# Kernel tuning notes

Hardware: AMD Instinct MI355X
Metric: run time of the kernel (lower is better)

The kernel has to match this reference:

```python
import jax, jax.numpy as jnp
import numpy as np
import math

D_MODEL = 1024
N_HEADS = 16
D_HEAD = D_MODEL // N_HEADS
NUM_BUCKETS = 32
MAX_DISTANCE = 128
B, LQ, LK = 2, 2048, 2048


def _rel_pos_bucket(rel):
    # rel: [Lq, Lk] int32, rel = mem - ctx
    n = jnp.clip(-rel, 0, None)
    max_exact = NUM_BUCKETS // 2
    is_small = n < max_exact
    val_if_large = max_exact + (
        jnp.log(n.astype(jnp.float32) / max_exact + 1e-9)
        / math.log(MAX_DISTANCE / max_exact)
        * (NUM_BUCKETS - max_exact)
    ).astype(jnp.int32)
    val_if_large = jnp.minimum(val_if_large, NUM_BUCKETS - 1)
    return jnp.where(is_small, n, val_if_large)


def setup_inputs() -> dict:
    key = jax.random.key(0)
    ks = jax.random.split(key, 9)
    scale = 1.0 / math.sqrt(D_MODEL)
    q = jax.random.normal(ks[0], (B, LQ, D_MODEL), dtype=jnp.float32)
    k = jax.random.normal(ks[1], (B, LK, D_MODEL), dtype=jnp.float32)
    v = jax.random.normal(ks[2], (B, LK, D_MODEL), dtype=jnp.float32)
    key_padding_mask = jax.random.randint(ks[3], (B, 1, 1, LK), 0, 2).astype(bool)
    Wq = jax.random.normal(ks[4], (D_MODEL, D_MODEL), dtype=jnp.float32) * scale
    Wk = jax.random.normal(ks[5], (D_MODEL, D_MODEL), dtype=jnp.float32) * scale
    Wv = jax.random.normal(ks[6], (D_MODEL, D_MODEL), dtype=jnp.float32) * scale
    Wo = jax.random.normal(ks[7], (D_MODEL, D_MODEL), dtype=jnp.float32) * scale
    rel_emb = jax.random.normal(ks[8], (NUM_BUCKETS, N_HEADS), dtype=jnp.float32) * 0.02
    return {"q": q, "k": k, "v": v, "key_padding_mask": key_padding_mask,
            "Wq": Wq, "Wk": Wk, "Wv": Wv, "Wo": Wo, "rel_emb": rel_emb}


def reference(q, k, v, key_padding_mask, Wq, Wk, Wv, Wo, rel_emb):
    Bq, Lq, _ = q.shape
    Lk = k.shape[1]
    # projections (nn.Linear: x @ W.T), split heads -> [B, H, L, dh]
    qh = (q @ Wq.T).reshape(Bq, Lq, N_HEADS, D_HEAD).transpose(0, 2, 1, 3)
    kh = (k @ Wk.T).reshape(Bq, Lk, N_HEADS, D_HEAD).transpose(0, 2, 1, 3)
    vh = (v @ Wv.T).reshape(Bq, Lk, N_HEADS, D_HEAD).transpose(0, 2, 1, 3)
    scores = jnp.einsum('bhqd,bhkd->bhqk', qh, kh) / math.sqrt(D_HEAD)
    # relative position bias: [1, H, Lq, Lk]
    rel = jnp.arange(Lk, dtype=jnp.int32)[None, :] - jnp.arange(Lq, dtype=jnp.int32)[:, None]
    buckets = _rel_pos_bucket(rel)  # [Lq, Lk]
    bias = rel_emb[buckets]         # [Lq, Lk, H]
    scores = scores + bias.transpose(2, 0, 1)[None]
    scores = jnp.where(key_padding_mask, scores, -1e9)
    attn = jax.nn.softmax(scores, axis=-1)
    out = jnp.einsum('bhqk,bhkd->bhqd', attn, vh)
    out = out.transpose(0, 2, 1, 3).reshape(Bq, Lq, D_MODEL)
    return out @ Wo.T
```

## Files before the change

kernel.cpp:

```cpp
#include <hip/hip_runtime.h>
#include <math.h>

typedef _Float16 f16;
typedef __fp16 h16x2 __attribute__((ext_vector_type(2)));
typedef _Float16 f16x4 __attribute__((ext_vector_type(4)));
typedef _Float16 f16x8 __attribute__((ext_vector_type(8)));
typedef float f32x4 __attribute__((ext_vector_type(4)));
typedef float f32x16 __attribute__((ext_vector_type(16)));
typedef unsigned int u32;

#define D_MODEL 1024
#define NHEADS 16
#define DHEAD 64
#define LQ 2048
#define LKK 2048
#define BB 2
#define LOG2E 1.4426950408889634f

static __device__ __forceinline__ void gload16(const void* g, void* l) {
  __builtin_amdgcn_global_load_lds(
      (const __attribute__((address_space(1))) u32*)g,
      (__attribute__((address_space(3))) u32*)l, 16, 0, 0);
}
static __device__ __forceinline__ float ex2(float x) {
  float r;
  asm volatile("v_exp_f32 %0, %1\n\ts_nop 0" : "=v"(r) : "v"(x));
  return r;
}
static __device__ __forceinline__ u32 pkr(float a, float b) {
  union { h16x2 h; u32 u; } c;
  c.h = __builtin_amdgcn_cvt_pkrtz(a, b);
  return c.u;
}
#define MFMA16(a, b, c) __builtin_amdgcn_mfma_f32_16x16x32_f16(a, b, c, 0, 0, 0)
#define MFMA32(a, b, c) __builtin_amdgcn_mfma_f32_32x32x16_f16(a, b, c, 0, 0, 0)

__global__ void k_prep(const void* msk, const float* __restrict__ rel,
                       float* __restrict__ biasT, unsigned char* __restrict__ m8) {
  __shared__ int o1s, o2s;
  const int t = threadIdx.x;
  if (t == 0) { o1s = 0; o2s = 0; }
  __syncthreads();
  const unsigned char* raw = (const unsigned char*)msk;
  int o1 = 0, o2 = 0;
  for (int i = t; i < BB * LKK; i += 256) {
    unsigned char vv = raw[i];
    if ((i & 3) && vv) o1 = 1;
    if (((i & 3) == 2) && vv == 0x80u) o2 = 1;
  }
  if (o1) atomicOr(&o1s, 1);
  if (o2) atomicOr(&o2s, 1);
  __syncthreads();
  const int f = o1s ? (o2s ? 2 : 1) : 0;
  for (int i = t; i < BB * LKK; i += 256) {
    unsigned char v;
    if (f == 0)      v = (((const int*)msk)[i] != 0);
    else if (f == 1) v = (((const unsigned char*)msk)[i] != 0);
    else             v = (((const float*)msk)[i] != 0.0f);
    m8[i] = v;
  }
  for (int n = t; n < 2048; n += 256) {
    int bucket;
    if (n < 16) bucket = n;
    else {
      float tt = logf((float)n / 16.0f + 1e-9f);
      tt = tt / 2.0794415416798357f;
      tt = tt * 16.0f;
      bucket = 16 + (int)tt;
      if (bucket > 31) bucket = 31;
    }
    for (int h = 0; h < NHEADS; ++h)
      biasT[h * 2048 + n] = rel[bucket * NHEADS + h] * LOG2E;
  }
}

__global__ void k_cvt_all(const float* q, const float* k, const float* v,
                          const float* Wq, const float* Wk, const float* Wv, const float* Wo,
                          f16* Xq, f16* Xk, f16* Xv, f16* W16) {
  int i = blockIdx.x * 256 + threadIdx.x;
  const float* s; f16* d; int off;
  if (i < 3145728) {
    int which = i >> 20; off = i & 1048575;
    s = which == 0 ? q : (which == 1 ? k : v);
    d = which == 0 ? Xq : (which == 1 ? Xk : Xv);
  } else {
    int j = i - 3145728; int which = j >> 18; off = j & 262143;
    s = which == 0 ? Wq : (which == 1 ? Wk : (which == 2 ? Wv : Wo));
    d = W16 + which * 1048576;
  }
  float4 x = ((const float4*)s)[off];
  f16x4 o; o[0] = (f16)x.x; o[1] = (f16)x.y; o[2] = (f16)x.z; o[3] = (f16)x.w;
  ((f16x4*)d)[off] = o;
}

template <int EPI>
static __device__ __forceinline__ void gemm_core(const f16* __restrict__ A,
                                                 const f16* __restrict__ Bm,
                                                 void* __restrict__ C) {
  __shared__ __align__(16) f16 sA[128 * 32];
  __shared__ __align__(16) f16 sB[128 * 32];
  const int t = threadIdx.x;
  const int w = t >> 6, lane = t & 63;
  const int lg = lane >> 4, lc = lane & 15;
  const int wr = w >> 1, wc = w & 1;
  const long row0 = (long)blockIdx.x * 128;
  const long col0 = (long)blockIdx.y * 128;
  f32x4 acc[4][4] = {};

  for (int kk = 0; kk < 1024; kk += 32) {
#pragma unroll
    for (int it = 0; it < 2; ++it) {
      int ch = t + it * 256;
      int r = ch >> 2, kg = ch & 3;
      gload16(A + (row0 + r) * 1024 + kk + kg * 8, (char*)sA + ch * 16);
      gload16(Bm + (col0 + r) * 1024 + kk + kg * 8, (char*)sB + ch * 16);
    }
    __syncthreads();
    f16x8 af[4], bf[4];
#pragma unroll
    for (int i = 0; i < 4; ++i)
      af[i] = *(const f16x8*)&sA[(wr * 64 + i * 16 + lc) * 32 + lg * 8];
#pragma unroll
    for (int j = 0; j < 4; ++j)
      bf[j] = *(const f16x8*)&sB[(wc * 64 + j * 16 + lc) * 32 + lg * 8];
#pragma unroll
    for (int i = 0; i < 4; ++i)
#pragma unroll
      for (int j = 0; j < 4; ++j)
        acc[i][j] = MFMA16(af[i], bf[j], acc[i][j]);
    __syncthreads();
  }
#pragma unroll
  for (int i = 0; i < 4; ++i)
#pragma unroll
    for (int j = 0; j < 4; ++j)
#pragma unroll
      for (int r = 0; r < 4; ++r) {
        long row = row0 + wr * 64 + i * 16 + lg * 4 + r;
        long col = col0 + wc * 64 + j * 16 + lc;
        float v = acc[i][j][r];
        if (EPI == 0) {
          long b = row >> 11, l = row & 2047;
          long h = col >> 6, d = col & 63;
          ((f16*)C)[(((b * NHEADS + h) * LQ) + l) * DHEAD + d] = (f16)v;
        } else {
          ((float*)C)[row * 1024 + col] = v;
        }
      }
}

__global__ void __launch_bounds__(256, 2)
k_gemm_qkv(const f16* __restrict__ Xq, const f16* __restrict__ Xk, const f16* __restrict__ Xv,
           const f16* __restrict__ W16, f16* __restrict__ QHp, f16* __restrict__ KHp,
           f16* __restrict__ VHp, int zoff) {
  const int z = blockIdx.z + zoff;
  const f16* A = z == 0 ? Xq : (z == 1 ? Xk : Xv);
  const f16* Bm = W16 + (size_t)z * 1048576;
  f16* C = z == 0 ? QHp : (z == 1 ? KHp : VHp);
  gemm_core<0>(A, Bm, C);
}

__global__ void __launch_bounds__(256, 2)
k_gemm_o(const f16* __restrict__ A, const f16* __restrict__ Bm, float* __restrict__ C) {
  gemm_core<1>(A, Bm, C);
}

__global__ void __launch_bounds__(256, 2)
k_attn(const f16* __restrict__ QH, const f16* __restrict__ KH, const f16* __restrict__ VH,
       const float* __restrict__ BIASg, const unsigned char* __restrict__ M8,
       f16* __restrict__ O16) {
  __shared__ __align__(16) f16 sK[2][64 * 64];
  __shared__ __align__(16) f16 sVT[2][64 * 64];
  __shared__ __align__(16) float sBias[4104];
  __shared__ __align__(16) float sPen[2048];

  const int L = blockIdx.x;
  const int bh = (L & 7) * 4 + ((L >> 3) & 3);
  const int qc = L >> 5;
  const int b = bh >> 4, h = bh & 15;
  const int t = threadIdx.x, w = t >> 6, lane = t & 63;
  const int lq = lane & 31;
  const int hi = lane >> 5;
  const int q0w = qc * 128 + w * 32;
  const size_t base = (size_t)bh * LKK * DHEAD;

  for (int i = t; i < 4104; i += 256) {
    int n = i - 2052; n = n < 0 ? 0 : (n > 2047 ? 2047 : n);
    sBias[i] = BIASg[h * 2048 + n];
  }
  for (int i = t; i < 2048; i += 256)
    sPen[i] = M8[b * LKK + i] ? 0.0f : -3.0e9f;

  f16x8 qb[4];
  const f16* qrow = QH + base + (size_t)(q0w + lq) * DHEAD;
#pragma unroll
  for (int s = 0; s < 4; ++s)
    qb[s] = *(const f16x8*)(qrow + s * 16 + hi * 8);

  auto STAGE = [&](int kt, int buf) {
#pragma unroll
    for (int it = 0; it < 2; ++it) {
      int ch = t + it * 256;
      int r = ch >> 3, g = ch & 7;
      gload16(KH + base + (size_t)(kt * 64 + r) * DHEAD + (g ^ (r & 7)) * 8,
              (char*)&sK[buf][0] + ch * 16);
    }
#pragma unroll
    for (int it = 0; it < 2; ++it) {
      int ch = t + it * 256;
      int kr = ch & 63, dg = ch >> 6;
      uint4 vv = *(const uint4*)(VH + base + (size_t)(kt * 64 + kr) * DHEAD + dg * 8);
      const f16* pv = (const f16*)&vv;
#pragma unroll
      for (int e = 0; e < 8; ++e) {
        int d = dg * 8 + e;
        *(f16*)((char*)&sVT[buf][0] + ((d * 128 + kr * 2) ^ ((d & 7) << 4))) = pv[e];
      }
    }
  };

  float m_r = -1e30f, l_r = 0.0f;
  f32x16 oacc0 = {}, oacc1 = {};
  const float c1 = 0.125f * LOG2E;

  STAGE(0, 0);
  __syncthreads();

  for (int kt = 0; kt < 32; ++kt) {
    const int cur = kt & 1;
    if (kt < 31) STAGE(kt + 1, cur ^ 1);

    f32x16 sa0 = {}, sa1 = {};
#pragma unroll
    for (int s = 0; s < 4; ++s) {
      f16x8 k0 = *(const f16x8*)((const char*)&sK[cur][0] +
                   ((lq * 128 + s * 32 + hi * 16) ^ ((lq & 7) << 4)));
      f16x8 k1 = *(const f16x8*)((const char*)&sK[cur][0] +
                   (((32 + lq) * 128 + s * 32 + hi * 16) ^ ((lq & 7) << 4)));
      sa0 = MFMA32(k0, qb[s], sa0);
      sa1 = MFMA32(k1, qb[s], sa1);
    }

    float p_[32];
#pragma unroll
    for (int r = 0; r < 16; ++r) { p_[r] = sa0[r]; p_[16 + r] = sa1[r]; }

#pragma unroll
    for (int u = 0; u < 8; ++u) {
      int tt = u >> 2, j = u & 3;
      int kbase = kt * 64 + tt * 32 + j * 8 + hi * 4;
      f32x4 pen4 = *(const f32x4*)&sPen[kbase];
      int bidx0 = (q0w + lq) - kbase + 2052;
#pragma unroll
      for (int e = 0; e < 4; ++e) {
        float bp = sBias[bidx0 - e] + pen4[e];
        int r = tt * 16 + j * 4 + e;
        p_[r] = p_[r] * c1 + bp;
      }
    }

    float tm[16];
#pragma unroll
    for (int r = 0; r < 16; ++r) tm[r] = fmaxf(p_[2 * r], p_[2 * r + 1]);
#pragma unroll
    for (int s = 8; s > 0; s >>= 1)
#pragma unroll
      for (int r = 0; r < s; ++r) tm[r] = fmaxf(tm[r], tm[r + s]);
    float mx = fmaxf(tm[0], __shfl_xor(tm[0], 32));

    if (__any(mx > m_r + 8.0f)) {
      float mnew = fmaxf(m_r, mx);
      float al = ex2(m_r - mnew);
      m_r = mnew; l_r *= al;
#pragma unroll
      for (int r = 0; r < 16; ++r) { oacc0[r] *= al; oacc1[r] *= al; }
    }

#pragma unroll
    for (int r = 0; r < 32; ++r) p_[r] = ex2(p_[r] - m_r);

    float ts[16];
#pragma unroll
    for (int r = 0; r < 16; ++r) ts[r] = p_[2 * r] + p_[2 * r + 1];
#pragma unroll
    for (int s = 8; s > 0; s >>= 1)
#pragma unroll
      for (int r = 0; r < s; ++r) ts[r] += ts[r + s];
    l_r += ts[0] + __shfl_xor(ts[0], 32);

    f16x8 pf[4];
#pragma unroll
    for (int sl = 0; sl < 4; ++sl) {
      int tt = sl >> 1, sp = sl & 1;
      int bA = tt * 16 + (2 * sp) * 4, bB = tt * 16 + (2 * sp + 1) * 4;
      u32 A0 = pkr(p_[bA], p_[bA + 1]);
      u32 A1 = pkr(p_[bA + 2], p_[bA + 3]);
      u32 B0 = pkr(p_[bB], p_[bB + 1]);
      u32 B1 = pkr(p_[bB + 2], p_[bB + 3]);
      asm volatile("v_permlane32_swap_b32 %0, %1" : "+v"(A0), "+v"(B0));
      asm volatile("v_permlane32_swap_b32 %0, %1" : "+v"(A1), "+v"(B1));
      union { u32 u[4]; f16x8 v; } c;
      c.u[0] = A0; c.u[1] = A1; c.u[2] = B0; c.u[3] = B1;
      pf[sl] = c.v;
    }

#pragma unroll
    for (int sl = 0; sl < 4; ++sl) {
      int K0 = sl * 16;
      f16x8 v0 = *(const f16x8*)((const char*)&sVT[cur][0] +
                   ((lq * 128 + K0 * 2 + hi * 16) ^ ((lq & 7) << 4)));
      f16x8 v1 = *(const f16x8*)((const char*)&sVT[cur][0] +
                   (((32 + lq) * 128 + K0 * 2 + hi * 16) ^ ((lq & 7) << 4)));
      oacc0 = MFMA32(v0, pf[sl], oacc0);
      oacc1 = MFMA32(v1, pf[sl], oacc1);
    }
    __syncthreads();
  }

  const float rinv = 1.0f / l_r;
  const size_t orow = ((size_t)b * LQ + (q0w + lq)) * D_MODEL + h * DHEAD;
#pragma unroll
  for (int dh = 0; dh < 2; ++dh)
#pragma unroll
    for (int j = 0; j < 4; ++j) {
      int d0 = dh * 32 + j * 8 + hi * 4;
      f16x4 ov;
#pragma unroll
      for (int e = 0; e < 4; ++e) {
        float x = (dh ? oacc1[j * 4 + e] : oacc0[j * 4 + e]) * rinv;
        ov[e] = (f16)x;
      }
      *(f16x4*)(O16 + orow + d0) = ov;
    }
}

extern "C" void kernel_launch(void* const* d_in, const int* in_sizes, int n_in,
                              void* d_out, int out_size, void* d_ws, size_t ws_size,
                              hipStream_t stream) {
  (void)in_sizes; (void)n_in; (void)out_size;
  const float* q   = (const float*)d_in[0];
  const float* k   = (const float*)d_in[1];
  const float* v   = (const float*)d_in[2];
  const void*  msk = d_in[3];
  const float* Wq  = (const float*)d_in[4];
  const float* Wk  = (const float*)d_in[5];
  const float* Wv  = (const float*)d_in[6];
  const float* Wo  = (const float*)d_in[7];
  const float* rel = (const float*)d_in[8];

  char* ws = (char*)d_ws;
  const size_t SL = (size_t)8 << 20;
  const bool bigA = ws_size >= 8 * SL;

  f16 *Xq, *Xk, *Xv, *QHp, *KHp, *VHp, *O16, *W16; char* misc;
  if (bigA) {
    Xq = (f16*)(ws + 0 * SL); Xk = (f16*)(ws + 1 * SL); Xv = (f16*)(ws + 2 * SL);
    QHp = (f16*)(ws + 3 * SL); KHp = (f16*)(ws + 4 * SL); VHp = (f16*)(ws + 5 * SL);
    W16 = (f16*)(ws + 6 * SL); O16 = (f16*)(ws + 2 * SL);
    misc = ws + 7 * SL;
  } else {
    Xq = (f16*)(ws + 0 * SL); Xk = (f16*)(ws + 1 * SL); Xv = (f16*)(ws + 2 * SL);
    QHp = (f16*)(ws + 3 * SL); KHp = (f16*)(ws + 0 * SL); VHp = (f16*)(ws + 1 * SL);
    W16 = (f16*)(ws + 4 * SL); O16 = (f16*)(ws + 2 * SL);
    misc = ws + 5 * SL;
  }
  float* BIAS = (float*)misc;
  unsigned char* M8 = (unsigned char*)(misc + (192 << 10));

  k_prep<<<1, 256, 0, stream>>>(msk, rel, BIAS, M8);
  k_cvt_all<<<16384, 256, 0, stream>>>(q, k, v, Wq, Wk, Wv, Wo, Xq, Xk, Xv, W16);

  if (bigA) {
    k_gemm_qkv<<<dim3(32, 8, 3), 256, 0, stream>>>(Xq, Xk, Xv, W16, QHp, KHp, VHp, 0);
  } else {
    for (int z = 0; z < 3; ++z)
      k_gemm_qkv<<<dim3(32, 8, 1), 256, 0, stream>>>(Xq, Xk, Xv, W16, QHp, KHp, VHp, z);
  }
  k_attn<<<512, 256, 0, stream>>>(QHp, KHp, VHp, BIAS, M8, O16);
  k_gemm_o<<<dim3(32, 8), 256, 0, stream>>>(O16, W16 + 3 * 1048576, (float*)d_out);
}
```

Baseline: 165.0 us.

## Write V projection pre-transposed and load it asynchronously into LDS

Result: faster. 155.1 us (-6.0%).

```diff
diff --git a/kernel.cpp b/kernel.cpp
--- a/kernel.cpp
+++ b/kernel.cpp
@@ -31,6 +31,9 @@
   union { h16x2 h; u32 u; } c;
   c.h = __builtin_amdgcn_cvt_pkrtz(a, b);
   return c.u;
+}
+static __device__ __forceinline__ float fmax3(float a, float b, float c) {
+  return fmaxf(fmaxf(a, b), c);
 }
 #define MFMA16(a, b, c) __builtin_amdgcn_mfma_f32_16x16x32_f16(a, b, c, 0, 0, 0)
 #define MFMA32(a, b, c) __builtin_amdgcn_mfma_f32_32x32x16_f16(a, b, c, 0, 0, 0)
@@ -133,31 +136,46 @@
 #pragma unroll
   for (int i = 0; i < 4; ++i)
 #pragma unroll
-    for (int j = 0; j < 4; ++j)
-#pragma unroll
-      for (int r = 0; r < 4; ++r) {
-        long row = row0 + wr * 64 + i * 16 + lg * 4 + r;
-        long col = col0 + wc * 64 + j * 16 + lc;
-        float v = acc[i][j][r];
-        if (EPI == 0) {
-          long b = row >> 11, l = row & 2047;
-          long h = col >> 6, d = col & 63;
-          ((f16*)C)[(((b * NHEADS + h) * LQ) + l) * DHEAD + d] = (f16)v;
-        } else {
-          ((float*)C)[row * 1024 + col] = v;
+    for (int j = 0; j < 4; ++j) {
+      const long rowb = row0 + wr * 64 + i * 16 + lg * 4;
+      const long col = col0 + wc * 64 + j * 16 + lc;
+      if (EPI == 2) {
+        long b = rowb >> 11, l0 = rowb & 2047;
+        long h = col >> 6, d = col & 63;
+        f16x4 ov;
+#pragma unroll
+        for (int r = 0; r < 4; ++r) ov[r] = (f16)acc[i][j][r];
+        *(f16x4*)((f16*)C + (((b * NHEADS + h) * DHEAD + d) * (long)LKK + l0)) = ov;
+      } else {
+#pragma unroll
+        for (int r = 0; r < 4; ++r) {
+          long row = rowb + r;
+          float v = acc[i][j][r];
+          if (EPI == 0) {
+            long b = row >> 11, l = row & 2047;
+            long h = col >> 6, d = col & 63;
+            ((f16*)C)[(((b * NHEADS + h) * LQ) + l) * DHEAD + d] = (f16)v;
+          } else {
+            ((float*)C)[row * 1024 + col] = v;
+          }
         }
       }
-}
-
-__global__ void __launch_bounds__(256, 2)
+    }
+}
+
+__global__ void __launch_bounds__(256, 3)
 k_gemm_qkv(const f16* __restrict__ Xq, const f16* __restrict__ Xk, const f16* __restrict__ Xv,
            const f16* __restrict__ W16, f16* __restrict__ QHp, f16* __restrict__ KHp,
-           f16* __restrict__ VHp, int zoff) {
+           f16* __restrict__ VTp, int zoff) {
   const int z = blockIdx.z + zoff;
-  const f16* A = z == 0 ? Xq : (z == 1 ? Xk : Xv);
-  const f16* Bm = W16 + (size_t)z * 1048576;
-  f16* C = z == 0 ? QHp : (z == 1 ? KHp : VHp);
-  gemm_core<0>(A, Bm, C);
+  if (z == 2) {
+    gemm_core<2>(Xv, W16 + 2 * 1048576, VTp);
+  } else {
+    const f16* A = z == 0 ? Xq : Xk;
+    const f16* Bm = W16 + (size_t)z * 1048576;
+    f16* C = z == 0 ? QHp : KHp;
+    gemm_core<0>(A, Bm, C);
+  }
 }
 
 __global__ void __launch_bounds__(256, 2)
@@ -166,7 +184,7 @@
 }
 
 __global__ void __launch_bounds__(256, 2)
-k_attn(const f16* __restrict__ QH, const f16* __restrict__ KH, const f16* __restrict__ VH,
+k_attn(const f16* __restrict__ QH, const f16* __restrict__ KH, const f16* __restrict__ VT,
        const float* __restrict__ BIASg, const unsigned char* __restrict__ M8,
        f16* __restrict__ O16) {
   __shared__ __align__(16) f16 sK[2][64 * 64];
@@ -197,31 +215,26 @@
   for (int s = 0; s < 4; ++s)
     qb[s] = *(const f16x8*)(qrow + s * 16 + hi * 8);
 
+  const int ch0 = t, ch1 = t + 256;
+  const int r0 = ch0 >> 3, g0 = ((ch0 & 7) ^ (r0 & 7)) * 8;
+  const int r1 = ch1 >> 3, g1 = ((ch1 & 7) ^ (r1 & 7)) * 8;
+  const f16* Kb = KH + base;
+  const f16* Vb = VT + base;
+
   auto STAGE = [&](int kt, int buf) {
-#pragma unroll
-    for (int it = 0; it < 2; ++it) {
-      int ch = t + it * 256;
-      int r = ch >> 3, g = ch & 7;
-      gload16(KH + base + (size_t)(kt * 64 + r) * DHEAD + (g ^ (r & 7)) * 8,
-              (char*)&sK[buf][0] + ch * 16);
-    }
-#pragma unroll
-    for (int it = 0; it < 2; ++it) {
-      int ch = t + it * 256;
-      int kr = ch & 63, dg = ch >> 6;
-      uint4 vv = *(const uint4*)(VH + base + (size_t)(kt * 64 + kr) * DHEAD + dg * 8);
-      const f16* pv = (const f16*)&vv;
-#pragma unroll
-      for (int e = 0; e < 8; ++e) {
-        int d = dg * 8 + e;
-        *(f16*)((char*)&sVT[buf][0] + ((d * 128 + kr * 2) ^ ((d & 7) << 4))) = pv[e];
-      }
-    }
+    const int k0 = kt * 64;
+    gload16(Kb + (size_t)(k0 + r0) * DHEAD + g0, (char*)&sK[buf][0] + ch0 * 16);
+    gload16(Kb + (size_t)(k0 + r1) * DHEAD + g1, (char*)&sK[buf][0] + ch1 * 16);
+    gload16(Vb + (size_t)r0 * LKK + k0 + g0, (char*)&sVT[buf][0] + ch0 * 16);
+    gload16(Vb + (size_t)r1 * LKK + k0 + g1, (char*)&sVT[buf][0] + ch1 * 16);
   };
 
-  float m_r = -1e30f, l_r = 0.0f;
-  f32x16 oacc0 = {}, oacc1 = {};
+  float m_r = -1e30f;
+  f32x16 oacc0 = {}, oacc1 = {}, oaccL = {};
   const float c1 = 0.125f * LOG2E;
+  f16x8 ones;
+#pragma unroll
+  for (int e = 0; e < 8; ++e) ones[e] = (f16)1.0f;
 
   STAGE(0, 0);
   __syncthreads();
@@ -259,34 +272,27 @@
       }
     }
 
-    float tm[16];
-#pragma unroll
-    for (int r = 0; r < 16; ++r) tm[r] = fmaxf(p_[2 * r], p_[2 * r + 1]);
-#pragma unroll
-    for (int s = 8; s > 0; s >>= 1)
-#pragma unroll
-      for (int r = 0; r < s; ++r) tm[r] = fmaxf(tm[r], tm[r + s]);
-    float mx = fmaxf(tm[0], __shfl_xor(tm[0], 32));
+    float mm[11];
+#pragma unroll
+    for (int r = 0; r < 10; ++r) mm[r] = fmax3(p_[3 * r], p_[3 * r + 1], p_[3 * r + 2]);
+    mm[10] = fmaxf(p_[30], p_[31]);
+    float a0 = fmax3(mm[0], mm[1], mm[2]);
+    float a1 = fmax3(mm[3], mm[4], mm[5]);
+    float a2 = fmax3(mm[6], mm[7], mm[8]);
+    float a3 = fmax3(mm[9], mm[10], a0);
+    float mx = fmax3(a1, a2, a3);
+    mx = fmaxf(mx, __shfl_xor(mx, 32));
 
     if (__any(mx > m_r + 8.0f)) {
       float mnew = fmaxf(m_r, mx);
       float al = ex2(m_r - mnew);
-      m_r = mnew; l_r *= al;
-#pragma unroll
-      for (int r = 0; r < 16; ++r) { oacc0[r] *= al; oacc1[r] *= al; }
+      m_r = mnew;
+#pragma unroll
+      for (int r = 0; r < 16; ++r) { oacc0[r] *= al; oacc1[r] *= al; oaccL[r] *= al; }
     }
 
 #pragma unroll
     for (int r = 0; r < 32; ++r) p_[r] = ex2(p_[r] - m_r);
-
-    float ts[16];
-#pragma unroll
-    for (int r = 0; r < 16; ++r) ts[r] = p_[2 * r] + p_[2 * r + 1];
-#pragma unroll
-    for (int s = 8; s > 0; s >>= 1)
-#pragma unroll
-      for (int r = 0; r < s; ++r) ts[r] += ts[r + s];
-    l_r += ts[0] + __shfl_xor(ts[0], 32);
 
     f16x8 pf[4];
 #pragma unroll
@@ -313,11 +319,12 @@
                    (((32 + lq) * 128 + K0 * 2 + hi * 16) ^ ((lq & 7) << 4)));
       oacc0 = MFMA32(v0, pf[sl], oacc0);
       oacc1 = MFMA32(v1, pf[sl], oacc1);
+      oaccL = MFMA32(ones, pf[sl], oaccL);
     }
     __syncthreads();
   }
 
-  const float rinv = 1.0f / l_r;
+  const float rinv = 1.0f / oaccL[0];
   const size_t orow = ((size_t)b * LQ + (q0w + lq)) * D_MODEL + h * DHEAD;
 #pragma unroll
   for (int dh = 0; dh < 2; ++dh)
@@ -352,15 +359,15 @@
   const size_t SL = (size_t)8 << 20;
   const bool bigA = ws_size >= 8 * SL;
 
-  f16 *Xq, *Xk, *Xv, *QHp, *KHp, *VHp, *O16, *W16; char* misc;
+  f16 *Xq, *Xk, *Xv, *QHp, *KHp, *VTp, *O16, *W16; char* misc;
   if (bigA) {
     Xq = (f16*)(ws + 0 * SL); Xk = (f16*)(ws + 1 * SL); Xv = (f16*)(ws + 2 * SL);
-    QHp = (f16*)(ws + 3 * SL); KHp = (f16*)(ws + 4 * SL); VHp = (f16*)(ws + 5 * SL);
+    QHp = (f16*)(ws + 3 * SL); KHp = (f16*)(ws + 4 * SL); VTp = (f16*)(ws + 5 * SL);
     W16 = (f16*)(ws + 6 * SL); O16 = (f16*)(ws + 2 * SL);
     misc = ws + 7 * SL;
   } else {
     Xq = (f16*)(ws + 0 * SL); Xk = (f16*)(ws + 1 * SL); Xv = (f16*)(ws + 2 * SL);
-    QHp = (f16*)(ws + 3 * SL); KHp = (f16*)(ws + 0 * SL); VHp = (f16*)(ws + 1 * SL);
+    QHp = (f16*)(ws + 3 * SL); KHp = (f16*)(ws + 0 * SL); VTp = (f16*)(ws + 1 * SL);
     W16 = (f16*)(ws + 4 * SL); O16 = (f16*)(ws + 2 * SL);
     misc = ws + 5 * SL;
   }
@@ -371,11 +378,11 @@
   k_cvt_all<<<16384, 256, 0, stream>>>(q, k, v, Wq, Wk, Wv, Wo, Xq, Xk, Xv, W16);
 
   if (bigA) {
-    k_gemm_qkv<<<dim3(32, 8, 3), 256, 0, stream>>>(Xq, Xk, Xv, W16, QHp, KHp, VHp, 0);
+    k_gemm_qkv<<<dim3(32, 8, 3), 256, 0, stream>>>(Xq, Xk, Xv, W16, QHp, KHp, VTp, 0);
   } else {
     for (int z = 0; z < 3; ++z)
-      k_gemm_qkv<<<dim3(32, 8, 1), 256, 0, stream>>>(Xq, Xk, Xv, W16, QHp, KHp, VHp, z);
-  }
-  k_attn<<<512, 256, 0, stream>>>(QHp, KHp, VHp, BIAS, M8, O16);
+      k_gemm_qkv<<<dim3(32, 8, 1), 256, 0, stream>>>(Xq, Xk, Xv, W16, QHp, KHp, VTp, z);
+  }
+  k_attn<<<512, 256, 0, stream>>>(QHp, KHp, VTp, BIAS, M8, O16);
   k_gemm_o<<<dim3(32, 8), 256, 0, stream>>>(O16, W16 + 3 * 1048576, (float*)d_out);
 }
```
